# Kernel optimization log

Measured on AMD Instinct MI355X. Metric: run time of the kernel, lower is better.

The kernel has to match this reference:

```python
import jax, jax.numpy as jnp
import numpy as np

HIDDEN = 2048
REDUCTION = 4
DOWN = HIDDEN // REDUCTION  # 512
E = 16
K = 2
B, S = 4, 2048


def setup_inputs() -> dict:
    key = jax.random.key(0)
    k1, k2, k3, k4 = jax.random.split(key, 4)
    x = jax.random.normal(k1, (B, S, HIDDEN), dtype=jnp.float32)
    gate_w = jax.random.normal(k2, (E, HIDDEN), dtype=jnp.float32) * 0.02
    # xavier_uniform over (E, DOWN, HIDDEN): bound = sqrt(6/(DOWN+HIDDEN))
    bound = float(np.sqrt(6.0 / (DOWN + HIDDEN)))
    down_w = jax.random.uniform(k3, (E, DOWN, HIDDEN), dtype=jnp.float32,
                                minval=-bound, maxval=bound)
    down_b = jnp.zeros((E, DOWN), dtype=jnp.float32)
    ub = float(np.sqrt(1.0 / DOWN))
    up_w = jax.random.uniform(k4, (HIDDEN, DOWN), dtype=jnp.float32,
                              minval=-ub, maxval=ub)
    up_b = jnp.zeros((HIDDEN,), dtype=jnp.float32)
    return {"x": x, "gate_w": gate_w, "down_w": down_w, "down_b": down_b,
            "up_w": up_w, "up_b": up_b}


def reference(x, gate_w, down_w, down_b, up_w, up_b):
    Bb, Ss, D = x.shape
    N = Bb * Ss
    xf = x.reshape(N, D)
    # TopKGate: logits -> top-k -> softmax over the k logits -> scatter to full [N,E]
    logits = xf @ gate_w.T                       # [N, E]
    topv, topi = jax.lax.top_k(logits, K)        # [N, K]
    probs = jax.nn.softmax(topv, axis=-1)        # [N, K]
    gw = jnp.zeros_like(logits).at[jnp.arange(N)[:, None], topi].set(probs)  # [N, E]
    # Dense-equivalent of gather + per-token bmm + scatter-add combine:
    # final[n] = sum_e gw[n,e] * (down_w[e] @ x[n] + down_b[e])
    expert_out = jnp.einsum('nd,eod->neo', xf, down_w) + down_b[None]  # [N, E, DOWN]
    combined = jnp.einsum('ne,neo->no', gw, expert_out)                # [N, DOWN]
    h = jax.nn.gelu(combined, approximate=True)  # gelu_new (tanh approx)
    h = h.reshape(Bb, Ss, DOWN)
    out = h @ up_w.T + up_b                      # [B, S, HIDDEN]
    # load balancing loss: E * sum(sum(gw,0)/N * mean(gw,0)) * alpha
    loss = E * jnp.sum(jnp.sum(gw, axis=0) / N * jnp.mean(gw, axis=0)) * 0.1
    return out, loss
```

## Files before the change

### kernel.cpp

```cpp
#include <hip/hip_runtime.h>
#include <hip/hip_bf16.h>
#include <math.h>

#define NTOK   8192
#define HID    2048
#define DWN    512
#define NEXP   16
#define PADSLOT 18432

#define OFF_XB       0
#define OFF_DWB      33554432
#define OFF_H        33554432
#define OFF_UWB      67108864
#define OFF_TOK      69206016
#define OFF_SPOS     69279744
#define OFF_EIDX     69345280
#define OFF_PVAL     69410816
#define OFF_COUNTS   69476352
#define OFF_BASE     69476416
#define OFF_CURSOR   69476544
#define OFF_COLSUM   69476608
#define OFF_SEG      69476672
#define SEGHALF_SHORTS 9437184
#define SEGHALF_BYTES  18874368
#define WS_NEED1     (OFF_SEG + 1 * SEGHALF_BYTES)
#define WS_NEED2     (OFF_SEG + 2 * SEGHALF_BYTES)

typedef __attribute__((ext_vector_type(8))) __bf16 bf16x8;
typedef __attribute__((ext_vector_type(4))) float f32x4;

#define ASYNC16(gsrc, ldst) \
  __builtin_amdgcn_global_load_lds((const __attribute__((address_space(1))) unsigned int*)(gsrc), \
                                   (__attribute__((address_space(3))) unsigned int*)(ldst), 16, 0, 0)

__device__ inline unsigned short f2bf(float f) {
  unsigned int u = __float_as_uint(f);
  unsigned int r = (u + 0x7FFFu + ((u >> 16) & 1u)) >> 16;
  return (unsigned short)r;
}
__device__ inline float bf2f(unsigned short s) {
  return __uint_as_float((unsigned int)s << 16);
}

__global__ __launch_bounds__(256) void cast8_kernel(const float* __restrict__ src,
                                                    unsigned short* __restrict__ dst)
{
  size_t i = ((size_t)blockIdx.x * 256 + threadIdx.x) * 8;
  float4 a = *(const float4*)(src + i);
  float4 b = *(const float4*)(src + i + 4);
  unsigned short o[8];
  o[0]=f2bf(a.x); o[1]=f2bf(a.y); o[2]=f2bf(a.z); o[3]=f2bf(a.w);
  o[4]=f2bf(b.x); o[5]=f2bf(b.y); o[6]=f2bf(b.z); o[7]=f2bf(b.w);
  *(uint4*)(dst + i) = *(const uint4*)o;
}

__global__ __launch_bounds__(256) void gate_kernel(
    const float* __restrict__ x, const float* __restrict__ gw,
    int2* __restrict__ eidx, float2* __restrict__ pvals)
{
  int lane = threadIdx.x & 63;
  int wave = threadIdx.x >> 6;
  int n = blockIdx.x * 4 + wave;
  const float* xr  = x + (size_t)n * HID;
  const float* gwp = gw + lane;

  double a0=0,a1=0,a2=0,a3=0,a4=0,a5=0,a6=0,a7=0;
  double a8=0,a9=0,a10=0,a11=0,a12=0,a13=0,a14=0,a15=0;

  for (int d0 = 0; d0 < HID; d0 += 64) {
    double xd = (double)xr[d0 + lane];
    const float* g = gwp + d0;
    a0  = fma(xd, (double)g[ 0*HID], a0);
    a1  = fma(xd, (double)g[ 1*HID], a1);
    a2  = fma(xd, (double)g[ 2*HID], a2);
    a3  = fma(xd, (double)g[ 3*HID], a3);
    a4  = fma(xd, (double)g[ 4*HID], a4);
    a5  = fma(xd, (double)g[ 5*HID], a5);
    a6  = fma(xd, (double)g[ 6*HID], a6);
    a7  = fma(xd, (double)g[ 7*HID], a7);
    a8  = fma(xd, (double)g[ 8*HID], a8);
    a9  = fma(xd, (double)g[ 9*HID], a9);
    a10 = fma(xd, (double)g[10*HID], a10);
    a11 = fma(xd, (double)g[11*HID], a11);
    a12 = fma(xd, (double)g[12*HID], a12);
    a13 = fma(xd, (double)g[13*HID], a13);
    a14 = fma(xd, (double)g[14*HID], a14);
    a15 = fma(xd, (double)g[15*HID], a15);
  }

#define RED(v) { v += __shfl_xor(v,32,64); v += __shfl_xor(v,16,64); v += __shfl_xor(v,8,64); \
                 v += __shfl_xor(v,4,64);  v += __shfl_xor(v,2,64);  v += __shfl_xor(v,1,64); }
  RED(a0) RED(a1) RED(a2) RED(a3) RED(a4) RED(a5) RED(a6) RED(a7)
  RED(a8) RED(a9) RED(a10) RED(a11) RED(a12) RED(a13) RED(a14) RED(a15)
#undef RED

  if (lane == 0) {
    double v0 = -1e300, v1 = -1e300;
    int i0 = 0, i1 = 0;
#define TOP(v,E) { if ((v) > v0) { v1 = v0; i1 = i0; v0 = (v); i0 = (E); } \
                   else if ((v) > v1) { v1 = (v); i1 = (E); } }
    TOP(a0,0) TOP(a1,1) TOP(a2,2) TOP(a3,3) TOP(a4,4) TOP(a5,5) TOP(a6,6) TOP(a7,7)
    TOP(a8,8) TOP(a9,9) TOP(a10,10) TOP(a11,11) TOP(a12,12) TOP(a13,13) TOP(a14,14) TOP(a15,15)
#undef TOP
    double ex = exp(v1 - v0);
    double denom = 1.0 + ex;
    eidx[n]  = make_int2(i0, i1);
    pvals[n] = make_float2((float)(1.0 / denom), (float)(ex / denom));
  }
}

__global__ __launch_bounds__(256) void hist_kernel(
    const int2* __restrict__ eidx, const float2* __restrict__ pvals,
    int* __restrict__ counts, float* __restrict__ colsum)
{
  __shared__ int   cbin[NEXP];
  __shared__ float lbin[NEXP];
  if (threadIdx.x < NEXP) { cbin[threadIdx.x] = 0; lbin[threadIdx.x] = 0.f; }
  __syncthreads();
  int n = blockIdx.x * 256 + threadIdx.x;
  int2 e = eidx[n];
  float2 p = pvals[n];
  atomicAdd(&cbin[e.x], 1);  atomicAdd(&lbin[e.x], p.x);
  atomicAdd(&cbin[e.y], 1);  atomicAdd(&lbin[e.y], p.y);
  __syncthreads();
  if (threadIdx.x < NEXP) {
    atomicAdd(&counts[threadIdx.x], cbin[threadIdx.x]);
    atomicAdd(&colsum[threadIdx.x], lbin[threadIdx.x]);
  }
}

__global__ void scan_loss_kernel(const int* __restrict__ counts, int* __restrict__ base,
                                 const float* __restrict__ colsum, float* __restrict__ loss_out)
{
  if (threadIdx.x == 0 && blockIdx.x == 0) {
    int acc = 0;
    for (int e = 0; e < NEXP; e++) { base[e] = acc; acc += (counts[e] + 127) & ~127; }
    base[NEXP] = acc;
    double s = 0.0;
    for (int e = 0; e < NEXP; e++) { double c = (double)colsum[e]; s += c * c; }
    loss_out[0] = (float)(1.6 * s / ((double)NTOK * (double)NTOK));
  }
}

__global__ __launch_bounds__(256) void scatter_kernel(
    const int2* __restrict__ eidx, const int* __restrict__ base, int* __restrict__ cursor,
    int* __restrict__ tok, int2* __restrict__ spos)
{
  int n = blockIdx.x * 256 + threadIdx.x;
  int lane = threadIdx.x & 63;
  int2 e = eidx[n];
  int myE[2] = {e.x, e.y};
  int myPos[2];
#pragma unroll
  for (int s = 0; s < 2; s++) {
    int eq = myE[s];
#pragma unroll
    for (int q = 0; q < NEXP; q++) {
      unsigned long long m = __ballot(eq == q);
      if (eq == q) {
        int cnt = __popcll(m);
        int pre = __popcll(m & ((1ull << lane) - 1ull));
        int b = 0;
        if (pre == 0) b = atomicAdd(&cursor[q], cnt);
        int leader = __ffsll((long long)m) - 1;
        b = __shfl(b, leader, 64);
        int pos = base[q] + b + pre;
        tok[pos] = n;
        myPos[s] = pos;
      }
    }
  }
  spos[n] = make_int2(myPos[0], myPos[1]);
}

__global__ __launch_bounds__(256) void down_mfma_kernel(
    const unsigned short* __restrict__ xb, const unsigned short* __restrict__ dwb,
    const int* __restrict__ base, const int* __restrict__ tok,
    unsigned short* __restrict__ seg, int kcount)
{
  __shared__ unsigned short smem[32768];

  int slot0 = blockIdx.x * 128;
  if (slot0 >= base[NEXP]) return;
  int e = 0;
#pragma unroll
  for (int q = 1; q < NEXP; q++) if (base[q] <= slot0) e = q;
  int out0 = blockIdx.y * 128;
  int kh   = blockIdx.z;
  int kbase = kh * kcount * 64;

  int tid = threadIdx.x;
  const int l = tid & 63, w = tid >> 6;
  const int wm = w & 1, wn = w >> 1;
  const int lm = l & 15, quad = l >> 4;

  const unsigned short* agp[4];
  const unsigned short* bgp[4];
#pragma unroll
  for (int i = 0; i < 4; i++) {
    int g = w * 4 + i;
    int r = g * 8 + (l & 7);
    int kc = l >> 3;
    int t = tok[slot0 + r];
    agp[i] = xb + (size_t)(t < 0 ? 0 : t) * HID + kbase + kc * 8;
    bgp[i] = dwb + ((size_t)e * DWN + out0 + r) * HID + kbase + kc * 8;
  }

  int am_off[4], bn_off[4];
#pragma unroll
  for (int mi = 0; mi < 4; mi++) {
    int m = wm * 64 + mi * 16 + lm;
    am_off[mi] = (m >> 3) * 512 + (m & 7) * 8 + quad * 64;
    int nn = wn * 64 + mi * 16 + lm;
    bn_off[mi] = (nn >> 3) * 512 + (nn & 7) * 8 + quad * 64;
  }

  f32x4 acc[4][4] = {};

#pragma unroll
  for (int i = 0; i < 4; i++) {
    int g = w * 4 + i;
    ASYNC16(agp[i], &smem[g * 512]);
    ASYNC16(bgp[i], &smem[8192 + g * 512]);
  }
  __syncthreads();

  int cur = 0;
  for (int it = 0; it < kcount; it++) {
    unsigned short* As = smem + cur * 16384;
    unsigned short* Bs = As + 8192;
    if (it + 1 < kcount) {
      int k0 = (it + 1) * 64;
      unsigned short* Ap = smem + (cur ^ 1) * 16384;
#pragma unroll
      for (int i = 0; i < 4; i++) {
        int g = w * 4 + i;
        ASYNC16(agp[i] + k0, &Ap[g * 512]);
        ASYNC16(bgp[i] + k0, &Ap[8192 + g * 512]);
      }
    }
#pragma unroll
    for (int kk = 0; kk < 2; kk++) {
      bf16x8 af[4], bfr[4];
#pragma unroll
      for (int mi = 0; mi < 4; mi++) af[mi]  = *(const bf16x8*)&As[am_off[mi] + kk * 256];
#pragma unroll
      for (int ni = 0; ni < 4; ni++) bfr[ni] = *(const bf16x8*)&Bs[bn_off[ni] + kk * 256];
#pragma unroll
      for (int mi = 0; mi < 4; mi++)
#pragma unroll
        for (int ni = 0; ni < 4; ni++)
          acc[mi][ni] = __builtin_amdgcn_mfma_f32_16x16x32_bf16(af[mi], bfr[ni], acc[mi][ni], 0, 0, 0);
    }
    __syncthreads();
    cur ^= 1;
  }

#pragma unroll
  for (int mi = 0; mi < 4; mi++)
#pragma unroll
    for (int reg = 0; reg < 4; reg++) {
      int m = wm * 64 + mi * 16 + quad * 4 + reg;
#pragma unroll
      for (int ni = 0; ni < 4; ni++) {
        int c = wn * 64 + ni * 16 + lm;
        smem[m * 136 + c] = f2bf(acc[mi][ni][reg]);
      }
    }
  __syncthreads();
#pragma unroll
  for (int it2 = 0; it2 < 8; it2++) {
    int chunk = it2 * 256 + tid;
    int row = chunk >> 4, off = (chunk & 15) * 8;
    uint4 v = *(const uint4*)&smem[row * 136 + off];
    *(uint4*)&seg[(size_t)kh * SEGHALF_SHORTS + (size_t)(slot0 + row) * 512 + out0 + off] = v;
  }
}

__global__ __launch_bounds__(256) void combine_gelu_kernel(
    const unsigned short* __restrict__ seg, const int2* __restrict__ spos,
    const float2* __restrict__ pv, const int2* __restrict__ eix,
    const float* __restrict__ db, unsigned short* __restrict__ h, int ksplit)
{
  int n = blockIdx.x * 4 + (threadIdx.x >> 6);
  int lane = threadIdx.x & 63;
  int c0 = lane * 8;
  int2 sp = spos[n];
  float2 p = pv[n];
  int2 e = eix[n];

  float d0[8] = {0,0,0,0,0,0,0,0}, d1[8] = {0,0,0,0,0,0,0,0};
  for (int hh = 0; hh < ksplit; hh++) {
    uint4 u0 = *(const uint4*)(seg + (size_t)hh * SEGHALF_SHORTS + (size_t)sp.x * 512 + c0);
    uint4 u1 = *(const uint4*)(seg + (size_t)hh * SEGHALF_SHORTS + (size_t)sp.y * 512 + c0);
    const unsigned short* s0 = (const unsigned short*)&u0;
    const unsigned short* s1 = (const unsigned short*)&u1;
#pragma unroll
    for (int j = 0; j < 8; j++) { d0[j] += bf2f(s0[j]); d1[j] += bf2f(s1[j]); }
  }
  float b0[8], b1[8];
  *(float4*)&b0[0] = *(const float4*)(db + e.x * DWN + c0);
  *(float4*)&b0[4] = *(const float4*)(db + e.x * DWN + c0 + 4);
  *(float4*)&b1[0] = *(const float4*)(db + e.y * DWN + c0);
  *(float4*)&b1[4] = *(const float4*)(db + e.y * DWN + c0 + 4);

  unsigned short o[8];
#pragma unroll
  for (int j = 0; j < 8; j++) {
    float xx = p.x * (d0[j] + b0[j]) + p.y * (d1[j] + b1[j]);
    float inner = 0.7978845608028654f * (xx + 0.044715f * xx * xx * xx);
    o[j] = f2bf(0.5f * xx * (1.0f + tanhf(inner)));
  }
  *(uint4*)(h + (size_t)n * DWN + c0) = *(const uint4*)o;
}

__global__ __launch_bounds__(256) void up_mfma_kernel(
    const unsigned short* __restrict__ h, const unsigned short* __restrict__ uwb,
    const float* __restrict__ ub, float* __restrict__ out)
{
  __shared__ unsigned short smem[32768];

  int row0 = blockIdx.x * 128;
  int col0 = blockIdx.y * 128;
  int tid = threadIdx.x;
  const int l = tid & 63, w = tid >> 6;
  const int wm = w & 1, wn = w >> 1;
  const int lm = l & 15, quad = l >> 4;

  const unsigned short* agp[4];
  const unsigned short* bgp[4];
#pragma unroll
  for (int i = 0; i < 4; i++) {
    int g = w * 4 + i;
    int r = g * 8 + (l & 7);
    int kc = l >> 3;
    agp[i] = h   + (size_t)(row0 + r) * DWN + kc * 8;
    bgp[i] = uwb + (size_t)(col0 + r) * DWN + kc * 8;
  }

  int am_off[4], bn_off[4];
#pragma unroll
  for (int mi = 0; mi < 4; mi++) {
    int m = wm * 64 + mi * 16 + lm;
    am_off[mi] = (m >> 3) * 512 + (m & 7) * 8 + quad * 64;
    int nn = wn * 64 + mi * 16 + lm;
    bn_off[mi] = (nn >> 3) * 512 + (nn & 7) * 8 + quad * 64;
  }

  f32x4 acc[4][4] = {};

#pragma unroll
  for (int i = 0; i < 4; i++) {
    int g = w * 4 + i;
    ASYNC16(agp[i], &smem[g * 512]);
    ASYNC16(bgp[i], &smem[8192 + g * 512]);
  }
  __syncthreads();

  int cur = 0;
  for (int k0 = 0; k0 < DWN; k0 += 64) {
    unsigned short* As = smem + cur * 16384;
    unsigned short* Bs = As + 8192;
    if (k0 + 64 < DWN) {
      unsigned short* Ap = smem + (cur ^ 1) * 16384;
#pragma unroll
      for (int i = 0; i < 4; i++) {
        int g = w * 4 + i;
        ASYNC16(agp[i] + k0 + 64, &Ap[g * 512]);
        ASYNC16(bgp[i] + k0 + 64, &Ap[8192 + g * 512]);
      }
    }
#pragma unroll
    for (int kk = 0; kk < 2; kk++) {
      bf16x8 af[4], bfr[4];
#pragma unroll
      for (int mi = 0; mi < 4; mi++) af[mi]  = *(const bf16x8*)&As[am_off[mi] + kk * 256];
#pragma unroll
      for (int ni = 0; ni < 4; ni++) bfr[ni] = *(const bf16x8*)&Bs[bn_off[ni] + kk * 256];
#pragma unroll
      for (int mi = 0; mi < 4; mi++)
#pragma unroll
        for (int ni = 0; ni < 4; ni++)
          acc[mi][ni] = __builtin_amdgcn_mfma_f32_16x16x32_bf16(af[mi], bfr[ni], acc[mi][ni], 0, 0, 0);
    }
    __syncthreads();
    cur ^= 1;
  }

  float ubv[4];
#pragma unroll
  for (int ni = 0; ni < 4; ni++)
    ubv[ni] = ub[col0 + wn * 64 + ni * 16 + lm];
#pragma unroll
  for (int mi = 0; mi < 4; mi++) {
#pragma unroll
    for (int reg = 0; reg < 4; reg++) {
      int m = row0 + wm * 64 + mi * 16 + quad * 4 + reg;
      float* orow = out + (size_t)m * HID;
#pragma unroll
      for (int ni = 0; ni < 4; ni++) {
        int gc = col0 + wn * 64 + ni * 16 + lm;
        orow[gc] = acc[mi][ni][reg] + ubv[ni];
      }
    }
  }
}

extern "C" void kernel_launch(void* const* d_in, const int* in_sizes, int n_in,
                              void* d_out, int out_size, void* d_ws, size_t ws_size,
                              hipStream_t stream)
{
  const float* x  = (const float*)d_in[0];
  const float* gw = (const float*)d_in[1];
  const float* dw = (const float*)d_in[2];
  const float* db = (const float*)d_in[3];
  const float* uw = (const float*)d_in[4];
  const float* ub = (const float*)d_in[5];
  float* out = (float*)d_out;

  char* ws = (char*)d_ws;
  unsigned short* xb   = (unsigned short*)(ws + OFF_XB);
  unsigned short* dwb  = (unsigned short*)(ws + OFF_DWB);
  unsigned short* uwb  = (unsigned short*)(ws + OFF_UWB);
  unsigned short* h    = (unsigned short*)(ws + OFF_H);
  unsigned short* seg  = (unsigned short*)(ws + OFF_SEG);
  int*    tok    = (int*)(ws + OFF_TOK);
  int2*   spos   = (int2*)(ws + OFF_SPOS);
  int2*   eidx   = (int2*)(ws + OFF_EIDX);
  float2* pvals  = (float2*)(ws + OFF_PVAL);
  int*    counts = (int*)(ws + OFF_COUNTS);
  int*    base   = (int*)(ws + OFF_BASE);
  int*    cursor = (int*)(ws + OFF_CURSOR);
  float*  colsum = (float*)(ws + OFF_COLSUM);

  const int ksplit = (ws_size >= (size_t)WS_NEED2) ? 2 : 1;
  const int kcount = (HID / 64) / ksplit;

  hipMemsetAsync(tok, 0xFF, PADSLOT * sizeof(int), stream);
  hipMemsetAsync(counts, 0, 320, stream);

  cast8_kernel<<<(NTOK * HID) / 8 / 256, 256, 0, stream>>>(x, xb);
  cast8_kernel<<<(NEXP * DWN * HID) / 8 / 256, 256, 0, stream>>>(dw, dwb);
  cast8_kernel<<<(HID * DWN) / 8 / 256, 256, 0, stream>>>(uw, uwb);

  gate_kernel<<<NTOK / 4, 256, 0, stream>>>(x, gw, eidx, pvals);
  hist_kernel<<<NTOK / 256, 256, 0, stream>>>(eidx, pvals, counts, colsum);
  scan_loss_kernel<<<1, 64, 0, stream>>>(counts, base, colsum, out + (size_t)NTOK * HID);
  scatter_kernel<<<NTOK / 256, 256, 0, stream>>>(eidx, base, cursor, tok, spos);

  dim3 gdown(PADSLOT / 128, DWN / 128, ksplit);
  down_mfma_kernel<<<gdown, 256, 0, stream>>>(xb, dwb, base, tok, seg, kcount);

  combine_gelu_kernel<<<NTOK / 4, 256, 0, stream>>>(seg, spos, pvals, eidx, db, h, ksplit);

  dim3 gup(NTOK / 128, HID / 128);
  up_mfma_kernel<<<gup, 256, 0, stream>>>(h, uwb, ub, out);
}
```

Before: 434.0 us.

## Fuse x bf16 cast into gate kernel and remap GEMM grids for XCD locality

Drops the standalone cast of x to bf16 and writes the bf16 copy from inside the gate kernel, which already reads every x element, so one full pass over the 64MB fp32 activation is removed. The down and up GEMM launches become 1D grids whose block index is remapped so that consecutive logical tiles land on the same XCD (8 XCDs, round-robin dispatch). The aim is better L2 reuse of shared expert weights and token rows. The gate kernel now also issues strided 2-byte stores, and the remap assumes the grid size divides evenly by 8.

```diff
diff --git a/kernel.cpp b/kernel.cpp
--- a/kernel.cpp
+++ b/kernel.cpp
@@ -7,6 +7,8 @@
 #define DWN    512
 #define NEXP   16
 #define PADSLOT 18432
+#define NSLOTBLK 144
+#define DGRID_HALF (NSLOTBLK * 4)
 
 #define OFF_XB       0
 #define OFF_DWB      33554432
@@ -56,19 +58,23 @@
 
 __global__ __launch_bounds__(256) void gate_kernel(
     const float* __restrict__ x, const float* __restrict__ gw,
-    int2* __restrict__ eidx, float2* __restrict__ pvals)
+    int2* __restrict__ eidx, float2* __restrict__ pvals,
+    unsigned short* __restrict__ xbw)
 {
   int lane = threadIdx.x & 63;
   int wave = threadIdx.x >> 6;
   int n = blockIdx.x * 4 + wave;
   const float* xr  = x + (size_t)n * HID;
+  unsigned short* xw = xbw + (size_t)n * HID;
   const float* gwp = gw + lane;
 
   double a0=0,a1=0,a2=0,a3=0,a4=0,a5=0,a6=0,a7=0;
   double a8=0,a9=0,a10=0,a11=0,a12=0,a13=0,a14=0,a15=0;
 
   for (int d0 = 0; d0 < HID; d0 += 64) {
-    double xd = (double)xr[d0 + lane];
+    float xv = xr[d0 + lane];
+    xw[d0 + lane] = f2bf(xv);
+    double xd = (double)xv;
     const float* g = gwp + d0;
     a0  = fma(xd, (double)g[ 0*HID], a0);
     a1  = fma(xd, (double)g[ 1*HID], a1);
@@ -180,13 +186,18 @@
 {
   __shared__ unsigned short smem[32768];
 
-  int slot0 = blockIdx.x * 128;
+  int wg  = blockIdx.x;
+  int cpx = gridDim.x >> 3;
+  int logical = (wg & 7) * cpx + (wg >> 3);
+  int kh      = logical / DGRID_HALF;
+  int r       = logical % DGRID_HALF;
+  int slot0   = (r >> 2) * 128;
+  int out0    = (r & 3) * 128;
+
   if (slot0 >= base[NEXP]) return;
   int e = 0;
 #pragma unroll
   for (int q = 1; q < NEXP; q++) if (base[q] <= slot0) e = q;
-  int out0 = blockIdx.y * 128;
-  int kh   = blockIdx.z;
   int kbase = kh * kcount * 64;
 
   int tid = threadIdx.x;
@@ -199,11 +210,11 @@
 #pragma unroll
   for (int i = 0; i < 4; i++) {
     int g = w * 4 + i;
-    int r = g * 8 + (l & 7);
+    int rr = g * 8 + (l & 7);
     int kc = l >> 3;
-    int t = tok[slot0 + r];
+    int t = tok[slot0 + rr];
     agp[i] = xb + (size_t)(t < 0 ? 0 : t) * HID + kbase + kc * 8;
-    bgp[i] = dwb + ((size_t)e * DWN + out0 + r) * HID + kbase + kc * 8;
+    bgp[i] = dwb + ((size_t)e * DWN + out0 + rr) * HID + kbase + kc * 8;
   }
 
   int am_off[4], bn_off[4];
@@ -320,8 +331,12 @@
 {
   __shared__ unsigned short smem[32768];
 
-  int row0 = blockIdx.x * 128;
-  int col0 = blockIdx.y * 128;
+  int wg  = blockIdx.x;
+  int cpx = gridDim.x >> 3;
+  int logical = (wg & 7) * cpx + (wg >> 3);
+  int row0 = (logical >> 4) * 128;
+  int col0 = (logical & 15) * 128;
+
   int tid = threadIdx.x;
   const int l = tid & 63, w = tid >> 6;
   const int wm = w & 1, wn = w >> 1;
@@ -332,10 +347,10 @@
 #pragma unroll
   for (int i = 0; i < 4; i++) {
     int g = w * 4 + i;
-    int r = g * 8 + (l & 7);
+    int rr = g * 8 + (l & 7);
     int kc = l >> 3;
-    agp[i] = h   + (size_t)(row0 + r) * DWN + kc * 8;
-    bgp[i] = uwb + (size_t)(col0 + r) * DWN + kc * 8;
+    agp[i] = h   + (size_t)(row0 + rr) * DWN + kc * 8;
+    bgp[i] = uwb + (size_t)(col0 + rr) * DWN + kc * 8;
   }
 
   int am_off[4], bn_off[4];
@@ -439,20 +454,17 @@
   hipMemsetAsync(tok, 0xFF, PADSLOT * sizeof(int), stream);
   hipMemsetAsync(counts, 0, 320, stream);
 
-  cast8_kernel<<<(NTOK * HID) / 8 / 256, 256, 0, stream>>>(x, xb);
   cast8_kernel<<<(NEXP * DWN * HID) / 8 / 256, 256, 0, stream>>>(dw, dwb);
   cast8_kernel<<<(HID * DWN) / 8 / 256, 256, 0, stream>>>(uw, uwb);
 
-  gate_kernel<<<NTOK / 4, 256, 0, stream>>>(x, gw, eidx, pvals);
+  gate_kernel<<<NTOK / 4, 256, 0, stream>>>(x, gw, eidx, pvals, xb);
   hist_kernel<<<NTOK / 256, 256, 0, stream>>>(eidx, pvals, counts, colsum);
   scan_loss_kernel<<<1, 64, 0, stream>>>(counts, base, colsum, out + (size_t)NTOK * HID);
   scatter_kernel<<<NTOK / 256, 256, 0, stream>>>(eidx, base, cursor, tok, spos);
 
-  dim3 gdown(PADSLOT / 128, DWN / 128, ksplit);
-  down_mfma_kernel<<<gdown, 256, 0, stream>>>(xb, dwb, base, tok, seg, kcount);
+  down_mfma_kernel<<<DGRID_HALF * ksplit, 256, 0, stream>>>(xb, dwb, base, tok, seg, kcount);
 
   combine_gelu_kernel<<<NTOK / 4, 256, 0, stream>>>(seg, spos, pvals, eidx, db, h, ksplit);
 
-  dim3 gup(NTOK / 128, HID / 128);
-  up_mfma_kernel<<<gup, 256, 0, stream>>>(h, uwb, ub, out);
-}
+  up_mfma_kernel<<<NTOK / 128 * (HID / 128), 256, 0, stream>>>(h, uwb, ub, out);
+}
```

Result: slower. 456.0 us (+5.1%).
